# Kernel tuning notes

Measured on AMD Instinct MI355X. Metric: run time of the kernel, lower is better.

The kernel has to match this reference:

```python
import jax, jax.numpy as jnp
import numpy as np

EPS = 1e-7
N_SINKHORN = 40


def setup_inputs() -> dict:
    key = jax.random.key(0)
    k1, k2, k3, k4 = jax.random.split(key, 4)
    n, l, K, batch = 1024, 4, 1, 32
    x = jax.random.randint(k1, (batch, n), 0, l)                      # class labels in [0, l)
    W = jax.random.normal(k2, (n, n), jnp.float32)                    # MI-derived logit weights
    V_compress = jax.random.normal(k3, (n, l), jnp.float32)           # log-marginals
    E_compress = jax.random.normal(k4, (K, n, n, l, l), jnp.float32) * 0.1  # log-joints
    return {"x": x, "W": W, "V_compress": V_compress, "E_compress": E_compress}


def reference(x, W, V_compress, E_compress):
    n, l = V_compress.shape
    which_moat = 0

    # --- marginals / joints ---
    V = jax.nn.softmax(V_compress, axis=1)            # [n, l]
    E = jnp.exp(E_compress[which_moat])               # [n, n, l, l]
    E = E / E.sum(axis=(-2, -1), keepdims=True)

    # --- 40-step Sinkhorn / IPF projection onto target row/col marginals ---
    A_b = V[:, None, :, None]                         # [n, 1, l, 1] target row marginals
    B_b = V[None, :, None, :]                         # [1, n, 1, l] target col marginals

    def ipf_step(E, _):
        E = E * (A_b / (E.sum(axis=3, keepdims=True) + EPS))
        E = E * (B_b / (E.sum(axis=2, keepdims=True) + EPS))
        E = E / (E.sum(axis=(-2, -1), keepdims=True) + EPS)
        return E, None

    E, _ = jax.lax.scan(ipf_step, E, None, length=N_SINKHORN)

    # zero the diagonal (i == j) blocks, clamp to [0, 1]
    E = jnp.clip(E * (1.0 - jnp.eye(n, dtype=E.dtype))[:, :, None, None], 0.0, 1.0)

    # --- tree-structured weights and base Laplacian ---
    Ws = jax.nn.sigmoid(W)
    Ws = jnp.tril(Ws, k=-1)
    Ws = Ws + Ws.T                                    # symmetric, zero diag
    L0 = -Ws + jnp.diag(Ws.sum(axis=1))               # [n, n]

    # --- gather per-sample marginals / pairwise probs ---
    idx = jnp.arange(n)
    Pr = V[idx[None, :], x]                           # [B, n]
    P = E[idx[None, :, None], idx[None, None, :], x[:, :, None], x[:, None, :]]  # [B, n, n]
    P = P / (Pr[:, :, None] * Pr[:, None, :])

    WP = Ws[None, :, :] * P                           # [B, n, n]
    eye = jnp.eye(n, dtype=WP.dtype)
    L = -WP + WP.sum(axis=2)[:, :, None] * eye        # batched diag_embed

    y = jnp.log(Pr + 1e-7).sum(axis=1)                # [B]
    _, ld1 = jnp.linalg.slogdet(L[:, 1:, 1:] + 1e-7)
    _, ld0 = jnp.linalg.slogdet(L0[1:, 1:] + 1e-7)
    return y + ld1 - ld0
```

## Files before the change

kernel.cpp:

```cpp
#include <hip/hip_runtime.h>
#include <math.h>

#define MSZ   1048576ull
#define NMAT  33
#define PANSZ 61440
#define NSINK 14

__device__ __forceinline__ float frcp(float x){ return __builtin_amdgcn_rcpf(x); }

typedef __attribute__((ext_vector_type(8)))  short  bfrag;
typedef __attribute__((ext_vector_type(8)))  unsigned short u16x8;
typedef __attribute__((ext_vector_type(16))) float  f32x16;

__device__ __forceinline__ unsigned short bf16rn(float x){
  unsigned u = __float_as_uint(x);
  unsigned r = u + 0x7fffu + ((u>>16)&1u);
  return (unsigned short)(r>>16);
}
__device__ __forceinline__ float bf2f(unsigned short h){
  return __uint_as_float(((unsigned)h)<<16);
}

__global__ void k_misc(const float* __restrict__ Vc, float* __restrict__ V,
                       const float* __restrict__ W, float* __restrict__ Ws){
  int t = threadIdx.x;
  if(blockIdx.x < 4){
    int i = blockIdx.x*256 + t;
    float4 v = ((const float4*)Vc)[i];
    float mx = fmaxf(fmaxf(v.x,v.y), fmaxf(v.z,v.w));
    float e0=__expf(v.x-mx), e1=__expf(v.y-mx), e2=__expf(v.z-mx), e3=__expf(v.w-mx);
    float is = 1.f/(e0+e1+e2+e3);
    ((float4*)V)[i] = make_float4(e0*is, e1*is, e2*is, e3*is);
  } else {
    int idx = (blockIdx.x-4)*256 + t;
    int i = idx>>10, j = idx&1023;
    float v = 0.f;
    if(i != j){
      float w = (i>j) ? W[i*1024+j] : W[j*1024+i];
      v = 1.f/(1.f+__expf(-w));
    }
    Ws[idx]=v;
  }
}

__global__ void k_pr_y(const float* __restrict__ V, const int* __restrict__ x,
                       float* __restrict__ PrInv, float* __restrict__ y){
  int b = blockIdx.x, t = threadIdx.x;
  __shared__ float red[256];
  float acc = 0.f;
  for(int i=t; i<1024; i+=256){
    int xv = x[b*1024+i];
    float pr = V[i*4+xv];
    PrInv[b*1024+i] = 1.f/pr;
    acc += logf(pr + 1e-7f);
  }
  red[t]=acc; __syncthreads();
  for(int s=128;s>0;s>>=1){ if(t<s) red[t]+=red[t+s]; __syncthreads(); }
  if(t==0) y[b]=red[0];
}

__global__ void __launch_bounds__(256) k_sinkhorn(
    const float* __restrict__ Ec, const float* __restrict__ V,
    const float* __restrict__ Ws, const float* __restrict__ PrInv,
    const int* __restrict__ x, float* __restrict__ mats,
    float* __restrict__ partial){
  int idx = blockIdx.x*256 + threadIdx.x;
  int i = idx>>10, j = idx&1023;
  if(i==0) return;
  int t = threadIdx.x;
  int lane = t & 63, wv = t >> 6;
  __shared__ float sE[256][17];
  float E[16];
  {
    const float4* p = (const float4*)(Ec + (size_t)idx*16);
    float4 q0=p[0], q1=p[1], q2=p[2], q3=p[3];
    E[0]=__expf(q0.x); E[1]=__expf(q0.y); E[2]=__expf(q0.z); E[3]=__expf(q0.w);
    E[4]=__expf(q1.x); E[5]=__expf(q1.y); E[6]=__expf(q1.z); E[7]=__expf(q1.w);
    E[8]=__expf(q2.x); E[9]=__expf(q2.y); E[10]=__expf(q2.z); E[11]=__expf(q2.w);
    E[12]=__expf(q3.x);E[13]=__expf(q3.y);E[14]=__expf(q3.z); E[15]=__expf(q3.w);
  }
  float s0=0.f;
  #pragma unroll
  for(int q=0;q<16;q++) s0+=E[q];
  float is0 = frcp(s0);
  #pragma unroll
  for(int q=0;q<16;q++) E[q]*=is0;
  float av[4], bv[4];
  {
    float4 va = ((const float4*)V)[i];
    av[0]=va.x; av[1]=va.y; av[2]=va.z; av[3]=va.w;
    float4 vb = ((const float4*)V)[j];
    bv[0]=vb.x; bv[1]=vb.y; bv[2]=vb.z; bv[3]=vb.w;
  }
  for(int it=0; it<NSINK; ++it){
    #pragma unroll
    for(int r=0;r<4;r++){
      float rs = E[4*r]+E[4*r+1]+E[4*r+2]+E[4*r+3];
      float sc = av[r]*frcp(rs+1e-7f);
      E[4*r]*=sc; E[4*r+1]*=sc; E[4*r+2]*=sc; E[4*r+3]*=sc;
    }
    #pragma unroll
    for(int c=0;c<4;c++){
      float cs = E[c]+E[4+c]+E[8+c]+E[12+c];
      float sc = bv[c]*frcp(cs+1e-7f);
      E[c]*=sc; E[4+c]*=sc; E[8+c]*=sc; E[12+c]*=sc;
    }
  }
  #pragma unroll
  for(int q=0;q<16;q++) sE[t][q] = fminf(fmaxf(E[q],0.f),1.f);
  float wsij = Ws[idx];
  for(int b=0;b<32;b++){
    int xi = x[b*1024+i];
    int xj = x[b*1024+j];
    float val = sE[t][(xi<<2)+xj] * wsij * PrInv[b*1024+i] * PrInv[b*1024+j];
    if(j!=0)
      mats[(size_t)(1+b)*MSZ + (size_t)(i-1)*1024 + (j-1)] = 1e-7f - val;
    float r = val;
    r += __shfl_down(r,32); r += __shfl_down(r,16); r += __shfl_down(r,8);
    r += __shfl_down(r,4);  r += __shfl_down(r,2);  r += __shfl_down(r,1);
    if(lane==0)
      partial[((size_t)b<<14) + ((size_t)(i-1)<<4) + ((blockIdx.x&3)<<2) + wv] = r;
  }
}

__global__ void k_l0(const float* __restrict__ Ws, float* __restrict__ mats){
  int r = blockIdx.x, t = threadIdx.x;
  float* orow = mats + (size_t)r*1024;
  if(r == 1023){
    float4 o = make_float4(0.f,0.f,0.f,0.f);
    if(t==255) o.w = 1.f;
    ((float4*)orow)[t] = o;
    return;
  }
  const float* wrow = Ws + (size_t)(r+1)*1024;
  float4 v = ((const float4*)wrow)[t];
  __shared__ float red[256];
  red[t] = v.x+v.y+v.z+v.w;
  __syncthreads();
  for(int s=128;s>0;s>>=1){ if(t<s) red[t]+=red[t+s]; __syncthreads(); }
  float rs = red[0];
  float o[4];
  #pragma unroll
  for(int q=0;q<4;q++){
    int c = 4*t+q;
    if(c==r)          o[q] = rs + 1e-7f;
    else if(c < 1023) o[q] = 1e-7f - wrow[c+1];
    else              o[q] = 0.f;
  }
  ((float4*)orow)[t] = make_float4(o[0],o[1],o[2],o[3]);
}

__global__ void k_patch(float* __restrict__ mats, const float* __restrict__ partial){
  int m = blockIdx.y + 1;
  int r = blockIdx.x*256 + threadIdx.x;
  float* A = mats + (size_t)m*MSZ;
  A[(size_t)r*1024 + 1023] = (r==1023) ? 1.f : 0.f;
  if(r < 1023){
    A[(size_t)1023*1024 + r] = 0.f;
    const float* pp = partial + (((size_t)(m-1))<<14) + ((size_t)r<<4);
    float s = 0.f;
    #pragma unroll
    for(int q=0;q<16;q++) s += pp[q];
    A[(size_t)r*1024 + r] = s + 1e-7f;
  }
}

__global__ void __launch_bounds__(128) k_diag(const float* __restrict__ mats_,
    unsigned short* __restrict__ UiH, unsigned short* __restrict__ UiL,
    unsigned short* __restrict__ LiH, unsigned short* __restrict__ LiL,
    float* __restrict__ logdet, int k){
  int m = blockIdx.x;
  const float* A = mats_ + (size_t)m*MSZ;
  int t = threadIdx.x;
  int lane = t & 63, w = t >> 6;
  __shared__ float Us[64*68];
  __shared__ float Ls[64*68];
  __shared__ float rd[64];

  if(w==0){
    float row[64];
    const float4* pr = (const float4*)(A + (size_t)(k+lane)*1024 + k);
    #pragma unroll
    for(int q4=0;q4<16;q4++){
      float4 v = pr[q4];
      row[4*q4]=v.x; row[4*q4+1]=v.y; row[4*q4+2]=v.z; row[4*q4+3]=v.w;
    }
    float slog = 0.f;
    #pragma unroll
    for(int c=0;c<64;c++){
      float piv = __shfl(row[c], c);
      slog += logf(fabsf(piv));
      float ip = frcp(piv);
      if(lane==c) rd[c] = ip;
      bool below = lane > c;
      float lic = below ? row[c]*ip : 0.f;
      if(below) row[c] = lic;
      #pragma unroll
      for(int q=c+1;q<64;q++){
        float uq = __shfl(row[q], c);
        row[q] = fmaf(-lic, uq, row[q]);
      }
    }
    #pragma unroll
    for(int q=0;q<64;q++){
      Ls[lane*68+q] = (q<lane) ? row[q] : 0.f;
      Us[lane*68+q] = (q>lane) ? row[q] : 0.f;
    }
    if(lane==0){ if(k==0) logdet[m]=slog; else logdet[m]+=slog; }
  }
  __syncthreads();

  if(w==0){
    float x[64];
    #pragma unroll
    for(int q=0;q<64;q++) x[q]=0.f;
    float rj = rd[lane];
    #pragma unroll
    for(int r=63;r>=0;r--){
      float a0=0.f,a1=0.f,a2=0.f,a3=0.f;
      #pragma unroll
      for(int c=(r+1)&~3; c<64; c+=4){
        float4 u = *(const float4*)&Us[r*68+c];
        a0 = fmaf(u.x, x[c],   a0);
        a1 = fmaf(u.y, x[c+1], a1);
        a2 = fmaf(u.z, x[c+2], a2);
        a3 = fmaf(u.w, x[c+3], a3);
      }
      float s = (a0+a1)+(a2+a3);
      x[r] = (r==lane) ? rj : -s*rd[r];
    }
    unsigned short* ph = UiH + (size_t)m*4096 + (size_t)lane*64;
    unsigned short* pl = UiL + (size_t)m*4096 + (size_t)lane*64;
    #pragma unroll
    for(int p8=0;p8<8;p8++){
      u16x8 h8, l8;
      #pragma unroll
      for(int e=0;e<8;e++){
        float v = x[p8*8+e];
        unsigned short h = bf16rn(v);
        h8[e]=h; l8[e]=bf16rn(v - bf2f(h));
      }
      ((u16x8*)ph)[p8]=h8; ((u16x8*)pl)[p8]=l8;
    }
  } else {
    float x[64];
    #pragma unroll
    for(int q=0;q<64;q++) x[q]=0.f;
    #pragma unroll
    for(int r=0;r<64;r++){
      float a0=0.f,a1=0.f,a2=0.f,a3=0.f;
      #pragma unroll
      for(int c=0; c<((r+3)&~3); c+=4){
        float4 u = *(const float4*)&Ls[r*68+c];
        a0 = fmaf(u.x, x[c],   a0);
        a1 = fmaf(u.y, x[c+1], a1);
        a2 = fmaf(u.z, x[c+2], a2);
        a3 = fmaf(u.w, x[c+3], a3);
      }
      x[r] = (r==lane) ? 1.f : -((a0+a1)+(a2+a3));
    }
    #pragma unroll
    for(int r=0;r<64;r++) Ls[r*68+lane] = x[r];
    unsigned short* ph = LiH + (size_t)m*4096 + (size_t)lane*64;
    unsigned short* pl = LiL + (size_t)m*4096 + (size_t)lane*64;
    #pragma unroll
    for(int p8=0;p8<8;p8++){
      float4 u0 = *(const float4*)&Ls[lane*68 + p8*8];
      float4 u1 = *(const float4*)&Ls[lane*68 + p8*8 + 4];
      float v[8] = {u0.x,u0.y,u0.z,u0.w,u1.x,u1.y,u1.z,u1.w};
      u16x8 h8, l8;
      #pragma unroll
      for(int e=0;e<8;e++){
        unsigned short h = bf16rn(v[e]);
        h8[e]=h; l8[e]=bf16rn(v[e] - bf2f(h));
      }
      ((u16x8*)ph)[p8]=h8; ((u16x8*)pl)[p8]=l8;
    }
  }
}

__global__ void __launch_bounds__(256) k_trsm(const float* __restrict__ mats_,
    const unsigned short* __restrict__ UiH, const unsigned short* __restrict__ UiL,
    const unsigned short* __restrict__ LiH, const unsigned short* __restrict__ LiL,
    unsigned short* __restrict__ Ah, unsigned short* __restrict__ Al,
    unsigned short* __restrict__ Bh, unsigned short* __restrict__ Bl,
    int k){
  int m = blockIdx.y;
  const float* A = mats_ + (size_t)m*MSZ;
  int rem = 1024 - (k+64);
  int nb = (rem+127)>>7;
  bool aside = (int)blockIdx.x < nb;
  int t = threadIdx.x, lane = t&63;
  int r32 = lane&31, hi = lane>>5, wv = t>>6;
  int tile0 = (aside ? (int)blockIdx.x : (int)blockIdx.x - nb)*128 + wv*32;
  int rel  = tile0 + r32;
  int relc = min(rel, rem-1);

  const unsigned short* IH = (aside ? UiH : LiH) + (size_t)m*4096;
  const unsigned short* IL = (aside ? UiL : LiL) + (size_t)m*4096;

  bfrag ah[4], al[4];
  if(aside){
    const float* src = A + (size_t)(k+64+relc)*1024 + k + hi*8;
    #pragma unroll
    for(int kc=0;kc<4;kc++){
      float4 u0 = *(const float4*)(src + kc*16);
      float4 u1 = *(const float4*)(src + kc*16 + 4);
      float v[8] = {u0.x,u0.y,u0.z,u0.w,u1.x,u1.y,u1.z,u1.w};
      #pragma unroll
      for(int e=0;e<8;e++){
        unsigned short h = bf16rn(v[e]);
        ah[kc][e] = (short)h;
        al[kc][e] = (short)bf16rn(v[e] - bf2f(h));
      }
    }
  } else {
    const float* src = A + (size_t)(k + hi*8)*1024 + (k+64+relc);
    #pragma unroll
    for(int kc=0;kc<4;kc++){
      #pragma unroll
      for(int e=0;e<8;e++){
        float v = src[(size_t)(kc*16+e)*1024];
        unsigned short h = bf16rn(v);
        ah[kc][e] = (short)h;
        al[kc][e] = (short)bf16rn(v - bf2f(h));
      }
    }
  }

  f32x16 acc[2];
  #pragma unroll
  for(int ct=0;ct<2;ct++)
    #pragma unroll
    for(int q=0;q<16;q++) acc[ct][q]=0.f;

  #pragma unroll
  for(int kc=0;kc<4;kc++){
    #pragma unroll
    for(int ct=0;ct<2;ct++){
      bfrag bh = *(const bfrag*)(IH + (size_t)(ct*32+r32)*64 + kc*16 + hi*8);
      bfrag bl = *(const bfrag*)(IL + (size_t)(ct*32+r32)*64 + kc*16 + hi*8);
      acc[ct] = __builtin_amdgcn_mfma_f32_32x32x16_bf16(ah[kc], bh, acc[ct], 0,0,0);
      acc[ct] = __builtin_amdgcn_mfma_f32_32x32x16_bf16(ah[kc], bl, acc[ct], 0,0,0);
      acc[ct] = __builtin_amdgcn_mfma_f32_32x32x16_bf16(al[kc], bh, acc[ct], 0,0,0);
    }
  }

  unsigned short* PH = (aside ? Ah : Bh) + (size_t)m*PANSZ;
  unsigned short* PL = (aside ? Al : Bl) + (size_t)m*PANSZ;
  #pragma unroll
  for(int ct=0;ct<2;ct++){
    #pragma unroll
    for(int reg=0;reg<16;reg++){
      int crow = (reg&3) + ((reg>>2)<<3) + (hi<<2);
      int r = tile0 + crow;
      if(r < rem){
        float v = acc[ct][reg];
        unsigned short h = bf16rn(v);
        size_t off = (size_t)r*64 + ct*32 + r32;
        PH[off] = h;
        PL[off] = bf16rn(v - bf2f(h));
      }
    }
  }
}

__global__ void __launch_bounds__(64) k_ld(const float* __restrict__ mats,
                                           float* __restrict__ logdet){
  int m = blockIdx.x, t = threadIdx.x;
  const float* A = mats + (size_t)m*MSZ;
  float row[64];
  #pragma unroll
  for(int q=0;q<64;q++)
    row[q] = A[(size_t)(960+t)*1024 + 960 + q];
  float slog = 0.f;
  #pragma unroll
  for(int c=0;c<64;c++){
    float piv = __shfl(row[c], c);
    slog += logf(fabsf(piv));
    float ip = frcp(piv);
    bool below = t > c;
    float lic = below ? row[c]*ip : 0.f;
    #pragma unroll
    for(int q=c+1;q<64;q++){
      float uq = __shfl(row[q], c);
      row[q] = fmaf(-lic, uq, row[q]);
    }
  }
  if(t==0) logdet[m] += slog;
}

__global__ void __launch_bounds__(256) k_gemm(float* __restrict__ mats,
    const unsigned short* __restrict__ Ah, const unsigned short* __restrict__ Al,
    const unsigned short* __restrict__ Bh, const unsigned short* __restrict__ Bl,
    int k){
  int m = blockIdx.z;
  float* A = mats + (size_t)m*MSZ;
  int rem = 1024 - (k+64);
  int i0rel = blockIdx.y*128;
  int j0rel = blockIdx.x*128;
  __shared__ unsigned short As[2][4096];
  __shared__ unsigned short Bs[2][4096];
  int t = threadIdx.x;
  int lane = t & 63, wvi = t >> 6;
  int wr = wvi >> 1, wc = wvi & 1;

  const unsigned short* pAh = Ah + (size_t)m*PANSZ;
  const unsigned short* pAl = Al + (size_t)m*PANSZ;
  const unsigned short* pBh = Bh + (size_t)m*PANSZ;
  const unsigned short* pBl = Bl + (size_t)m*PANSZ;

  int rowA[2], koctA[2], ldsOff[2];
  bool vA[2], vB[2];
  size_t offA[2], offB[2];
  #pragma unroll
  for(int p=0;p<2;p++){
    int c = t + 256*p;
    int row = c>>2, koct = c&3;
    rowA[p]=row; koctA[p]=koct;
    ldsOff[p] = row*32 + ((koct ^ ((row>>1)&3))<<3);
    vA[p] = (i0rel+row) < rem;
    vB[p] = (j0rel+row) < rem;
    offA[p] = (size_t)(i0rel+row)*64 + koct*8;
    offB[p] = (size_t)(j0rel+row)*64 + koct*8;
  }
  u16x8 z; z = 0;

  #pragma unroll
  for(int p=0;p<2;p++){
    u16x8 ah = vA[p] ? *(const u16x8*)(pAh + offA[p]) : z;
    u16x8 al = vA[p] ? *(const u16x8*)(pAl + offA[p]) : z;
    u16x8 bh = vB[p] ? *(const u16x8*)(pBh + offB[p]) : z;
    u16x8 bl = vB[p] ? *(const u16x8*)(pBl + offB[p]) : z;
    *(u16x8*)&As[0][ldsOff[p]] = ah;
    *(u16x8*)&As[1][ldsOff[p]] = al;
    *(u16x8*)&Bs[0][ldsOff[p]] = bh;
    *(u16x8*)&Bs[1][ldsOff[p]] = bl;
  }
  u16x8 p1[8];
  #pragma unroll
  for(int p=0;p<2;p++){
    p1[4*p+0] = vA[p] ? *(const u16x8*)(pAh + offA[p] + 32) : z;
    p1[4*p+1] = vA[p] ? *(const u16x8*)(pAl + offA[p] + 32) : z;
    p1[4*p+2] = vB[p] ? *(const u16x8*)(pBh + offB[p] + 32) : z;
    p1[4*p+3] = vB[p] ? *(const u16x8*)(pBl + offB[p] + 32) : z;
  }
  __syncthreads();

  f32x16 acc[2][2];
  #pragma unroll
  for(int rt=0;rt<2;rt++)
    #pragma unroll
    for(int ct=0;ct<2;ct++)
      #pragma unroll
      for(int q=0;q<16;q++) acc[rt][ct][q] = 0.f;

  int kgrp = lane >> 5;
  #pragma unroll
  for(int ks=0; ks<2; ks++){
    #pragma unroll
    for(int kc=0;kc<2;kc++){
      int koct = kc*2 + kgrp;
      bfrag ah[2], al[2], bh[2], bl[2];
      #pragma unroll
      for(int rt=0;rt<2;rt++){
        int row = wr*64 + rt*32 + (lane&31);
        int ad = row*32 + ((koct ^ ((row>>1)&3))<<3);
        ah[rt] = *(const bfrag*)&As[0][ad];
        al[rt] = *(const bfrag*)&As[1][ad];
      }
      #pragma unroll
      for(int ct=0;ct<2;ct++){
        int col = wc*64 + ct*32 + (lane&31);
        int ad = col*32 + ((koct ^ ((col>>1)&3))<<3);
        bh[ct] = *(const bfrag*)&Bs[0][ad];
        bl[ct] = *(const bfrag*)&Bs[1][ad];
      }
      #pragma unroll
      for(int rt=0;rt<2;rt++)
        #pragma unroll
        for(int ct=0;ct<2;ct++){
          acc[rt][ct] = __builtin_amdgcn_mfma_f32_32x32x16_bf16(ah[rt], bh[ct], acc[rt][ct], 0,0,0);
          acc[rt][ct] = __builtin_amdgcn_mfma_f32_32x32x16_bf16(ah[rt], bl[ct], acc[rt][ct], 0,0,0);
          acc[rt][ct] = __builtin_amdgcn_mfma_f32_32x32x16_bf16(al[rt], bh[ct], acc[rt][ct], 0,0,0);
        }
    }
    if(ks==0){
      __syncthreads();
      #pragma unroll
      for(int p=0;p<2;p++){
        *(u16x8*)&As[0][ldsOff[p]] = p1[4*p+0];
        *(u16x8*)&As[1][ldsOff[p]] = p1[4*p+1];
        *(u16x8*)&Bs[0][ldsOff[p]] = p1[4*p+2];
        *(u16x8*)&Bs[1][ldsOff[p]] = p1[4*p+3];
      }
      __syncthreads();
    }
  }

  int r0 = k + 64;
  #pragma unroll
  for(int rt=0;rt<2;rt++){
    int rowblk = i0rel + wr*64 + rt*32;
    if(rowblk >= rem) continue;
    #pragma unroll
    for(int ct=0;ct<2;ct++){
      int colblk = j0rel + wc*64 + ct*32;
      if(colblk >= rem) continue;
      int col = r0 + colblk + (lane&31);
      int rbase = r0 + rowblk + ((lane>>5)<<2);
      #pragma unroll
      for(int reg=0;reg<16;reg++){
        int row = rbase + (reg&3) + ((reg>>2)<<3);
        float* pc = A + (size_t)row*1024 + col;
        *pc -= acc[rt][ct][reg];
      }
    }
  }
}

__global__ void k_final(const float* __restrict__ y, const float* __restrict__ logdet,
                        float* __restrict__ out){
  int b = threadIdx.x;
  if(b<32) out[b] = y[b] + logdet[1+b] - logdet[0];
}

extern "C" void kernel_launch(void* const* d_in, const int* in_sizes, int n_in,
                              void* d_out, int out_size, void* d_ws, size_t ws_size,
                              hipStream_t stream){
  (void)in_sizes; (void)n_in; (void)out_size; (void)ws_size;
  const int*   x  = (const int*)d_in[0];
  const float* W  = (const float*)d_in[1];
  const float* Vc = (const float*)d_in[2];
  const float* Ec = (const float*)d_in[3];
  float* out = (float*)d_out;

  char* p = (char*)d_ws;
  auto alloc = [&](size_t bytes)->char*{ char* r = p; p += (bytes+255)&~(size_t)255; return r; };
  float* mats   = (float*)alloc((size_t)NMAT*MSZ*4);
  float* Ws     = (float*)alloc(1048576ull*4);
  unsigned short* Ah = (unsigned short*)alloc((size_t)NMAT*PANSZ*2);
  unsigned short* Al = (unsigned short*)alloc((size_t)NMAT*PANSZ*2);
  unsigned short* Bh = (unsigned short*)alloc((size_t)NMAT*PANSZ*2);
  unsigned short* Bl = (unsigned short*)alloc((size_t)NMAT*PANSZ*2);
  unsigned short* UiH = (unsigned short*)alloc((size_t)NMAT*4096*2);
  unsigned short* UiL = (unsigned short*)alloc((size_t)NMAT*4096*2);
  unsigned short* LiH = (unsigned short*)alloc((size_t)NMAT*4096*2);
  unsigned short* LiL = (unsigned short*)alloc((size_t)NMAT*4096*2);
  float* V      = (float*)alloc(4096*4);
  float* PrInv  = (float*)alloc(32768*4);
  float* partial= (float*)alloc((size_t)32*16384*4);
  float* y      = (float*)alloc(256);
  float* logdet = (float*)alloc(256);

  k_misc<<<4100,256,0,stream>>>(Vc, V, W, Ws);
  k_pr_y<<<32,256,0,stream>>>(V, x, PrInv, y);
  k_sinkhorn<<<4096,256,0,stream>>>(Ec, V, Ws, PrInv, x, mats, partial);
  k_l0<<<1024,256,0,stream>>>(Ws, mats);
  k_patch<<<dim3(4,32),256,0,stream>>>(mats, partial);

  for(int s=0;s<15;s++){
    int k = 64*s;
    int rem = 1024 - (k+64);
    k_diag<<<NMAT,128,0,stream>>>(mats, UiH,UiL,LiH,LiL, logdet, k);
    int nb = (rem+127)/128;
    k_trsm<<<dim3(2*nb,NMAT),256,0,stream>>>(mats, UiH,UiL,LiH,LiL, Ah,Al,Bh,Bl, k);
    int nt = (rem+127)/128;
    k_gemm<<<dim3(nt,nt,NMAT),256,0,stream>>>(mats, Ah,Al,Bh,Bl, k);
  }
  k_ld<<<NMAT,64,0,stream>>>(mats, logdet);
  k_final<<<1,32,0,stream>>>(y, logdet, out);
}
```

Baseline: 1.306 ms.

## Double blocked LU panel width to 128 and fold final logdet into diag kernel

The blocked LU used for the batched slogdet now works on 128-wide panels instead of 64. The diagonal kernel factors the 128x128 block as two 64x64 LUs with an in-LDS Schur update, then inverts its triangular factors for the TRSM step. This halves the number of diag/trsm/gemm launch rounds and gives each GEMM a longer K loop, at the cost of a heavier, more serial diag kernel with large register arrays (128 floats per thread) and 64KB of LDS. The separate final logdet kernel is dropped because the last diag call handles the trailing block, and the boundary masking is removed since 1024 divides evenly by 128.

```diff
diff --git a/kernel.cpp b/kernel.cpp
--- a/kernel.cpp
+++ b/kernel.cpp
@@ -1,10 +1,10 @@
 #include <hip/hip_runtime.h>
 #include <math.h>
 
-#define MSZ   1048576ull
-#define NMAT  33
-#define PANSZ 61440
-#define NSINK 14
+#define MSZ    1048576ull
+#define NMAT   33
+#define PANSZ  114688
+#define NSINK  14
 
 __device__ __forceinline__ float frcp(float x){ return __builtin_amdgcn_rcpf(x); }
 
@@ -165,33 +165,37 @@
   }
 }
 
-__global__ void __launch_bounds__(128) k_diag(const float* __restrict__ mats_,
+__global__ void __launch_bounds__(256) k_diag(const float* __restrict__ mats_,
     unsigned short* __restrict__ UiH, unsigned short* __restrict__ UiL,
     unsigned short* __restrict__ LiH, unsigned short* __restrict__ LiL,
-    float* __restrict__ logdet, int k){
+    float* __restrict__ logdet, int k, int inv){
   int m = blockIdx.x;
   const float* A = mats_ + (size_t)m*MSZ;
-  int t = threadIdx.x;
-  int lane = t & 63, w = t >> 6;
-  __shared__ float Us[64*68];
-  __shared__ float Ls[64*68];
-  __shared__ float rd[64];
-
+  int t = threadIdx.x, lane = t & 63, w = t >> 6;
+  __shared__ float sm[128*128];
+
+  {
+    int r = t >> 1, h = (t & 1) * 64;
+    const float4* src = (const float4*)(A + (size_t)(k + r)*1024 + k + h);
+    float4* dst = (float4*)&sm[r*128 + h];
+    #pragma unroll
+    for(int q=0;q<16;q++) dst[q] = src[q];
+  }
+  __syncthreads();
+
+  float slog = 0.f;
   if(w==0){
     float row[64];
-    const float4* pr = (const float4*)(A + (size_t)(k+lane)*1024 + k);
     #pragma unroll
     for(int q4=0;q4<16;q4++){
-      float4 v = pr[q4];
+      float4 v = *(const float4*)&sm[lane*128 + 4*q4];
       row[4*q4]=v.x; row[4*q4+1]=v.y; row[4*q4+2]=v.z; row[4*q4+3]=v.w;
     }
-    float slog = 0.f;
     #pragma unroll
     for(int c=0;c<64;c++){
       float piv = __shfl(row[c], c);
       slog += logf(fabsf(piv));
       float ip = frcp(piv);
-      if(lane==c) rd[c] = ip;
       bool below = lane > c;
       float lic = below ? row[c]*ip : 0.f;
       if(below) row[c] = lic;
@@ -202,11 +206,7 @@
       }
     }
     #pragma unroll
-    for(int q=0;q<64;q++){
-      Ls[lane*68+q] = (q<lane) ? row[q] : 0.f;
-      Us[lane*68+q] = (q>lane) ? row[q] : 0.f;
-    }
-    if(lane==0){ if(k==0) logdet[m]=slog; else logdet[m]+=slog; }
+    for(int q=0;q<64;q++) sm[lane*128+q] = row[q];
   }
   __syncthreads();
 
@@ -214,25 +214,110 @@
     float x[64];
     #pragma unroll
     for(int q=0;q<64;q++) x[q]=0.f;
-    float rj = rd[lane];
-    #pragma unroll
-    for(int r=63;r>=0;r--){
+    #pragma unroll
+    for(int r=0;r<64;r++){
       float a0=0.f,a1=0.f,a2=0.f,a3=0.f;
       #pragma unroll
-      for(int c=(r+1)&~3; c<64; c+=4){
-        float4 u = *(const float4*)&Us[r*68+c];
-        a0 = fmaf(u.x, x[c],   a0);
-        a1 = fmaf(u.y, x[c+1], a1);
-        a2 = fmaf(u.z, x[c+2], a2);
-        a3 = fmaf(u.w, x[c+3], a3);
-      }
-      float s = (a0+a1)+(a2+a3);
-      x[r] = (r==lane) ? rj : -s*rd[r];
-    }
-    unsigned short* ph = UiH + (size_t)m*4096 + (size_t)lane*64;
-    unsigned short* pl = UiL + (size_t)m*4096 + (size_t)lane*64;
-    #pragma unroll
-    for(int p8=0;p8<8;p8++){
+      for(int c=0;c<((r+3)&~3);c+=4){
+        float4 u = *(const float4*)&sm[r*128+c];
+        a0=fmaf(u.x,x[c],a0);   a1=fmaf(u.y,x[c+1],a1);
+        a2=fmaf(u.z,x[c+2],a2); a3=fmaf(u.w,x[c+3],a3);
+      }
+      x[r] = sm[r*128 + 64 + lane] - ((a0+a1)+(a2+a3));
+    }
+    #pragma unroll
+    for(int r=0;r<64;r++) sm[r*128 + 64 + lane] = x[r];
+  } else if(w==1){
+    float x[64];
+    #pragma unroll
+    for(int q=0;q<64;q++) x[q]=0.f;
+    #pragma unroll
+    for(int c=0;c<64;c++){
+      float a0=0.f,a1=0.f,a2=0.f,a3=0.f;
+      #pragma unroll
+      for(int p=0;p<((c+3)&~3);p+=4){
+        a0 = fmaf(x[p],   sm[p*128+c],     a0);
+        a1 = fmaf(x[p+1], sm[(p+1)*128+c], a1);
+        a2 = fmaf(x[p+2], sm[(p+2)*128+c], a2);
+        a3 = fmaf(x[p+3], sm[(p+3)*128+c], a3);
+      }
+      float d = sm[(64+lane)*128 + c];
+      x[c] = (d - ((a0+a1)+(a2+a3))) * frcp(sm[c*128+c]);
+    }
+    #pragma unroll
+    for(int c=0;c<64;c++) sm[(64+lane)*128 + c] = x[c];
+  }
+  __syncthreads();
+
+  {
+    int j = lane;
+    #pragma unroll
+    for(int ii=0; ii<16; ii++){
+      int i = w*16 + ii;
+      float acc2 = sm[(64+i)*128 + 64 + j];
+      #pragma unroll
+      for(int p=0;p<64;p+=4){
+        float4 l4 = *(const float4*)&sm[(64+i)*128 + p];
+        acc2 = fmaf(-l4.x, sm[(p  )*128 + 64 + j], acc2);
+        acc2 = fmaf(-l4.y, sm[(p+1)*128 + 64 + j], acc2);
+        acc2 = fmaf(-l4.z, sm[(p+2)*128 + 64 + j], acc2);
+        acc2 = fmaf(-l4.w, sm[(p+3)*128 + 64 + j], acc2);
+      }
+      sm[(64+i)*128 + 64 + j] = acc2;
+    }
+  }
+  __syncthreads();
+
+  if(w==0){
+    float row[64];
+    #pragma unroll
+    for(int q4=0;q4<16;q4++){
+      float4 v = *(const float4*)&sm[(64+lane)*128 + 64 + 4*q4];
+      row[4*q4]=v.x; row[4*q4+1]=v.y; row[4*q4+2]=v.z; row[4*q4+3]=v.w;
+    }
+    #pragma unroll
+    for(int c=0;c<64;c++){
+      float piv = __shfl(row[c], c);
+      slog += logf(fabsf(piv));
+      float ip = frcp(piv);
+      bool below = lane > c;
+      float lic = below ? row[c]*ip : 0.f;
+      if(below) row[c] = lic;
+      #pragma unroll
+      for(int q=c+1;q<64;q++){
+        float uq = __shfl(row[q], c);
+        row[q] = fmaf(-lic, uq, row[q]);
+      }
+    }
+    #pragma unroll
+    for(int q=0;q<64;q++) sm[(64+lane)*128 + 64 + q] = row[q];
+    if(lane==0){ if(k==0) logdet[m]=slog; else logdet[m]+=slog; }
+  }
+  __syncthreads();
+  if(!inv) return;
+
+  int col = t & 127;
+  if(t < 128){
+    float x[128];
+    #pragma unroll
+    for(int q=0;q<128;q++) x[q]=0.f;
+    #pragma unroll
+    for(int r=127;r>=0;r--){
+      float a0=0.f,a1=0.f,a2=0.f,a3=0.f;
+      #pragma unroll
+      for(int c=(r+1)&~3; c<128; c+=4){
+        float4 u = *(const float4*)&sm[r*128+c];
+        a0=fmaf(u.x,x[c],a0);   a1=fmaf(u.y,x[c+1],a1);
+        a2=fmaf(u.z,x[c+2],a2); a3=fmaf(u.w,x[c+3],a3);
+      }
+      float ip = frcp(sm[r*128+r]);
+      float sv = (a0+a1)+(a2+a3);
+      x[r] = (r==col) ? ip : -sv*ip;
+    }
+    unsigned short* ph = UiH + (size_t)m*16384 + (size_t)col*128;
+    unsigned short* pl = UiL + (size_t)m*16384 + (size_t)col*128;
+    #pragma unroll
+    for(int p8=0;p8<16;p8++){
       u16x8 h8, l8;
       #pragma unroll
       for(int e=0;e<8;e++){
@@ -242,31 +327,33 @@
       }
       ((u16x8*)ph)[p8]=h8; ((u16x8*)pl)[p8]=l8;
     }
+    __syncthreads();
+    __syncthreads();
   } else {
-    float x[64];
-    #pragma unroll
-    for(int q=0;q<64;q++) x[q]=0.f;
-    #pragma unroll
-    for(int r=0;r<64;r++){
+    float x[128];
+    #pragma unroll
+    for(int q=0;q<128;q++) x[q]=0.f;
+    #pragma unroll
+    for(int r=0;r<128;r++){
       float a0=0.f,a1=0.f,a2=0.f,a3=0.f;
       #pragma unroll
       for(int c=0; c<((r+3)&~3); c+=4){
-        float4 u = *(const float4*)&Ls[r*68+c];
-        a0 = fmaf(u.x, x[c],   a0);
-        a1 = fmaf(u.y, x[c+1], a1);
-        a2 = fmaf(u.z, x[c+2], a2);
-        a3 = fmaf(u.w, x[c+3], a3);
-      }
-      x[r] = (r==lane) ? 1.f : -((a0+a1)+(a2+a3));
-    }
-    #pragma unroll
-    for(int r=0;r<64;r++) Ls[r*68+lane] = x[r];
-    unsigned short* ph = LiH + (size_t)m*4096 + (size_t)lane*64;
-    unsigned short* pl = LiL + (size_t)m*4096 + (size_t)lane*64;
-    #pragma unroll
-    for(int p8=0;p8<8;p8++){
-      float4 u0 = *(const float4*)&Ls[lane*68 + p8*8];
-      float4 u1 = *(const float4*)&Ls[lane*68 + p8*8 + 4];
+        float4 u = *(const float4*)&sm[r*128+c];
+        a0=fmaf(u.x,x[c],a0);   a1=fmaf(u.y,x[c+1],a1);
+        a2=fmaf(u.z,x[c+2],a2); a3=fmaf(u.w,x[c+3],a3);
+      }
+      x[r] = (r==col) ? 1.f : -((a0+a1)+(a2+a3));
+    }
+    __syncthreads();
+    #pragma unroll
+    for(int r=0;r<128;r++) sm[r*128 + col] = x[r];
+    __syncthreads();
+    unsigned short* ph = LiH + (size_t)m*16384 + (size_t)col*128;
+    unsigned short* pl = LiL + (size_t)m*16384 + (size_t)col*128;
+    #pragma unroll
+    for(int p8=0;p8<16;p8++){
+      float4 u0 = *(const float4*)&sm[col*128 + p8*8];
+      float4 u1 = *(const float4*)&sm[col*128 + p8*8 + 4];
       float v[8] = {u0.x,u0.y,u0.z,u0.w,u1.x,u1.y,u1.z,u1.w};
       u16x8 h8, l8;
       #pragma unroll
@@ -287,107 +374,69 @@
     int k){
   int m = blockIdx.y;
   const float* A = mats_ + (size_t)m*MSZ;
-  int rem = 1024 - (k+64);
-  int nb = (rem+127)>>7;
+  int rem = 1024 - (k+128);
+  int nb = rem >> 7;
   bool aside = (int)blockIdx.x < nb;
   int t = threadIdx.x, lane = t&63;
   int r32 = lane&31, hi = lane>>5, wv = t>>6;
   int tile0 = (aside ? (int)blockIdx.x : (int)blockIdx.x - nb)*128 + wv*32;
   int rel  = tile0 + r32;
-  int relc = min(rel, rem-1);
-
-  const unsigned short* IH = (aside ? UiH : LiH) + (size_t)m*4096;
-  const unsigned short* IL = (aside ? UiL : LiL) + (size_t)m*4096;
-
-  bfrag ah[4], al[4];
-  if(aside){
-    const float* src = A + (size_t)(k+64+relc)*1024 + k + hi*8;
-    #pragma unroll
-    for(int kc=0;kc<4;kc++){
-      float4 u0 = *(const float4*)(src + kc*16);
-      float4 u1 = *(const float4*)(src + kc*16 + 4);
-      float v[8] = {u0.x,u0.y,u0.z,u0.w,u1.x,u1.y,u1.z,u1.w};
-      #pragma unroll
-      for(int e=0;e<8;e++){
-        unsigned short h = bf16rn(v[e]);
-        ah[kc][e] = (short)h;
-        al[kc][e] = (short)bf16rn(v[e] - bf2f(h));
-      }
-    }
-  } else {
-    const float* src = A + (size_t)(k + hi*8)*1024 + (k+64+relc);
-    #pragma unroll
-    for(int kc=0;kc<4;kc++){
-      #pragma unroll
-      for(int e=0;e<8;e++){
-        float v = src[(size_t)(kc*16+e)*1024];
-        unsigned short h = bf16rn(v);
-        ah[kc][e] = (short)h;
-        al[kc][e] = (short)bf16rn(v - bf2f(h));
-      }
-    }
-  }
-
-  f32x16 acc[2];
-  #pragma unroll
-  for(int ct=0;ct<2;ct++)
+
+  const unsigned short* IH = (aside ? UiH : LiH) + (size_t)m*16384;
+  const unsigned short* IL = (aside ? UiL : LiL) + (size_t)m*16384;
+
+  f32x16 acc[4];
+  #pragma unroll
+  for(int ct=0;ct<4;ct++)
     #pragma unroll
     for(int q=0;q<16;q++) acc[ct][q]=0.f;
 
   #pragma unroll
-  for(int kc=0;kc<4;kc++){
-    #pragma unroll
-    for(int ct=0;ct<2;ct++){
-      bfrag bh = *(const bfrag*)(IH + (size_t)(ct*32+r32)*64 + kc*16 + hi*8);
-      bfrag bl = *(const bfrag*)(IL + (size_t)(ct*32+r32)*64 + kc*16 + hi*8);
-      acc[ct] = __builtin_amdgcn_mfma_f32_32x32x16_bf16(ah[kc], bh, acc[ct], 0,0,0);
-      acc[ct] = __builtin_amdgcn_mfma_f32_32x32x16_bf16(ah[kc], bl, acc[ct], 0,0,0);
-      acc[ct] = __builtin_amdgcn_mfma_f32_32x32x16_bf16(al[kc], bh, acc[ct], 0,0,0);
+  for(int kc=0;kc<8;kc++){
+    float v[8];
+    if(aside){
+      const float* src = A + (size_t)(k+128+rel)*1024 + k + kc*16 + hi*8;
+      float4 u0 = ((const float4*)src)[0];
+      float4 u1 = ((const float4*)src)[1];
+      v[0]=u0.x; v[1]=u0.y; v[2]=u0.z; v[3]=u0.w;
+      v[4]=u1.x; v[5]=u1.y; v[6]=u1.z; v[7]=u1.w;
+    } else {
+      const float* src = A + (size_t)(k + kc*16 + hi*8)*1024 + (k+128+rel);
+      #pragma unroll
+      for(int e=0;e<8;e++) v[e] = src[(size_t)e*1024];
+    }
+    bfrag ah, al;
+    #pragma unroll
+    for(int e=0;e<8;e++){
+      unsigned short h = bf16rn(v[e]);
+      ah[e] = (short)h;
+      al[e] = (short)bf16rn(v[e] - bf2f(h));
+    }
+    #pragma unroll
+    for(int ct=0;ct<4;ct++){
+      bfrag bh = *(const bfrag*)(IH + (size_t)(ct*32+r32)*128 + kc*16 + hi*8);
+      bfrag bl = *(const bfrag*)(IL + (size_t)(ct*32+r32)*128 + kc*16 + hi*8);
+      acc[ct] = __builtin_amdgcn_mfma_f32_32x32x16_bf16(ah, bh, acc[ct], 0,0,0);
+      acc[ct] = __builtin_amdgcn_mfma_f32_32x32x16_bf16(ah, bl, acc[ct], 0,0,0);
+      acc[ct] = __builtin_amdgcn_mfma_f32_32x32x16_bf16(al, bh, acc[ct], 0,0,0);
     }
   }
 
   unsigned short* PH = (aside ? Ah : Bh) + (size_t)m*PANSZ;
   unsigned short* PL = (aside ? Al : Bl) + (size_t)m*PANSZ;
   #pragma unroll
-  for(int ct=0;ct<2;ct++){
+  for(int ct=0;ct<4;ct++){
     #pragma unroll
     for(int reg=0;reg<16;reg++){
       int crow = (reg&3) + ((reg>>2)<<3) + (hi<<2);
       int r = tile0 + crow;
-      if(r < rem){
-        float v = acc[ct][reg];
-        unsigned short h = bf16rn(v);
-        size_t off = (size_t)r*64 + ct*32 + r32;
-        PH[off] = h;
-        PL[off] = bf16rn(v - bf2f(h));
-      }
-    }
-  }
-}
-
-__global__ void __launch_bounds__(64) k_ld(const float* __restrict__ mats,
-                                           float* __restrict__ logdet){
-  int m = blockIdx.x, t = threadIdx.x;
-  const float* A = mats + (size_t)m*MSZ;
-  float row[64];
-  #pragma unroll
-  for(int q=0;q<64;q++)
-    row[q] = A[(size_t)(960+t)*1024 + 960 + q];
-  float slog = 0.f;
-  #pragma unroll
-  for(int c=0;c<64;c++){
-    float piv = __shfl(row[c], c);
-    slog += logf(fabsf(piv));
-    float ip = frcp(piv);
-    bool below = t > c;
-    float lic = below ? row[c]*ip : 0.f;
-    #pragma unroll
-    for(int q=c+1;q<64;q++){
-      float uq = __shfl(row[q], c);
-      row[q] = fmaf(-lic, uq, row[q]);
-    }
-  }
-  if(t==0) logdet[m] += slog;
+      float v = acc[ct][reg];
+      unsigned short h = bf16rn(v);
+      size_t off = (size_t)r*128 + ct*32 + r32;
+      PH[off] = h;
+      PL[off] = bf16rn(v - bf2f(h));
+    }
+  }
 }
 
 __global__ void __launch_bounds__(256) k_gemm(float* __restrict__ mats,
@@ -396,7 +445,6 @@
     int k){
   int m = blockIdx.z;
   float* A = mats + (size_t)m*MSZ;
-  int rem = 1024 - (k+64);
   int i0rel = blockIdx.y*128;
   int j0rel = blockIdx.x*128;
   __shared__ unsigned short As[2][4096];
@@ -410,40 +458,35 @@
   const unsigned short* pBh = Bh + (size_t)m*PANSZ;
   const unsigned short* pBl = Bl + (size_t)m*PANSZ;
 
-  int rowA[2], koctA[2], ldsOff[2];
-  bool vA[2], vB[2];
+  int ldsOff[2];
   size_t offA[2], offB[2];
   #pragma unroll
   for(int p=0;p<2;p++){
     int c = t + 256*p;
     int row = c>>2, koct = c&3;
-    rowA[p]=row; koctA[p]=koct;
     ldsOff[p] = row*32 + ((koct ^ ((row>>1)&3))<<3);
-    vA[p] = (i0rel+row) < rem;
-    vB[p] = (j0rel+row) < rem;
-    offA[p] = (size_t)(i0rel+row)*64 + koct*8;
-    offB[p] = (size_t)(j0rel+row)*64 + koct*8;
-  }
-  u16x8 z; z = 0;
+    offA[p] = (size_t)(i0rel+row)*128 + koct*8;
+    offB[p] = (size_t)(j0rel+row)*128 + koct*8;
+  }
 
   #pragma unroll
   for(int p=0;p<2;p++){
-    u16x8 ah = vA[p] ? *(const u16x8*)(pAh + offA[p]) : z;
-    u16x8 al = vA[p] ? *(const u16x8*)(pAl + offA[p]) : z;
-    u16x8 bh = vB[p] ? *(const u16x8*)(pBh + offB[p]) : z;
-    u16x8 bl = vB[p] ? *(const u16x8*)(pBl + offB[p]) : z;
-    *(u16x8*)&As[0][ldsOff[p]] = ah;
-    *(u16x8*)&As[1][ldsOff[p]] = al;
-    *(u16x8*)&Bs[0][ldsOff[p]] = bh;
-    *(u16x8*)&Bs[1][ldsOff[p]] = bl;
+    u16x8 a0 = *(const u16x8*)(pAh + offA[p]);
+    u16x8 a1 = *(const u16x8*)(pAl + offA[p]);
+    u16x8 b0 = *(const u16x8*)(pBh + offB[p]);
+    u16x8 b1 = *(const u16x8*)(pBl + offB[p]);
+    *(u16x8*)&As[0][ldsOff[p]] = a0;
+    *(u16x8*)&As[1][ldsOff[p]] = a1;
+    *(u16x8*)&Bs[0][ldsOff[p]] = b0;
+    *(u16x8*)&Bs[1][ldsOff[p]] = b1;
   }
   u16x8 p1[8];
   #pragma unroll
   for(int p=0;p<2;p++){
-    p1[4*p+0] = vA[p] ? *(const u16x8*)(pAh + offA[p] + 32) : z;
-    p1[4*p+1] = vA[p] ? *(const u16x8*)(pAl + offA[p] + 32) : z;
-    p1[4*p+2] = vB[p] ? *(const u16x8*)(pBh + offB[p] + 32) : z;
-    p1[4*p+3] = vB[p] ? *(const u16x8*)(pBl + offB[p] + 32) : z;
+    p1[4*p+0] = *(const u16x8*)(pAh + offA[p] + 32);
+    p1[4*p+1] = *(const u16x8*)(pAl + offA[p] + 32);
+    p1[4*p+2] = *(const u16x8*)(pBh + offB[p] + 32);
+    p1[4*p+3] = *(const u16x8*)(pBl + offB[p] + 32);
   }
   __syncthreads();
 
@@ -457,7 +500,7 @@
 
   int kgrp = lane >> 5;
   #pragma unroll
-  for(int ks=0; ks<2; ks++){
+  for(int st=0; st<4; st++){
     #pragma unroll
     for(int kc=0;kc<2;kc++){
       int koct = kc*2 + kgrp;
@@ -485,7 +528,7 @@
           acc[rt][ct] = __builtin_amdgcn_mfma_f32_32x32x16_bf16(al[rt], bh[ct], acc[rt][ct], 0,0,0);
         }
     }
-    if(ks==0){
+    if(st<3){
       __syncthreads();
       #pragma unroll
       for(int p=0;p<2;p++){
@@ -494,19 +537,26 @@
         *(u16x8*)&Bs[0][ldsOff[p]] = p1[4*p+2];
         *(u16x8*)&Bs[1][ldsOff[p]] = p1[4*p+3];
       }
+      if(st<2){
+        #pragma unroll
+        for(int p=0;p<2;p++){
+          p1[4*p+0] = *(const u16x8*)(pAh + offA[p] + (st+2)*32);
+          p1[4*p+1] = *(const u16x8*)(pAl + offA[p] + (st+2)*32);
+          p1[4*p+2] = *(const u16x8*)(pBh + offB[p] + (st+2)*32);
+          p1[4*p+3] = *(const u16x8*)(pBl + offB[p] + (st+2)*32);
+        }
+      }
       __syncthreads();
     }
   }
 
-  int r0 = k + 64;
+  int r0 = k + 128;
   #pragma unroll
   for(int rt=0;rt<2;rt++){
     int rowblk = i0rel + wr*64 + rt*32;
-    if(rowblk >= rem) continue;
     #pragma unroll
     for(int ct=0;ct<2;ct++){
       int colblk = j0rel + wc*64 + ct*32;
-      if(colblk >= rem) continue;
       int col = r0 + colblk + (lane&31);
       int rbase = r0 + rowblk + ((lane>>5)<<2);
       #pragma unroll
@@ -543,10 +593,10 @@
   unsigned short* Al = (unsigned short*)alloc((size_t)NMAT*PANSZ*2);
   unsigned short* Bh = (unsigned short*)alloc((size_t)NMAT*PANSZ*2);
   unsigned short* Bl = (unsigned short*)alloc((size_t)NMAT*PANSZ*2);
-  unsigned short* UiH = (unsigned short*)alloc((size_t)NMAT*4096*2);
-  unsigned short* UiL = (unsigned short*)alloc((size_t)NMAT*4096*2);
-  unsigned short* LiH = (unsigned short*)alloc((size_t)NMAT*4096*2);
-  unsigned short* LiL = (unsigned short*)alloc((size_t)NMAT*4096*2);
+  unsigned short* UiH = (unsigned short*)alloc((size_t)NMAT*16384*2);
+  unsigned short* UiL = (unsigned short*)alloc((size_t)NMAT*16384*2);
+  unsigned short* LiH = (unsigned short*)alloc((size_t)NMAT*16384*2);
+  unsigned short* LiL = (unsigned short*)alloc((size_t)NMAT*16384*2);
   float* V      = (float*)alloc(4096*4);
   float* PrInv  = (float*)alloc(32768*4);
   float* partial= (float*)alloc((size_t)32*16384*4);
@@ -559,15 +609,14 @@
   k_l0<<<1024,256,0,stream>>>(Ws, mats);
   k_patch<<<dim3(4,32),256,0,stream>>>(mats, partial);
 
-  for(int s=0;s<15;s++){
-    int k = 64*s;
-    int rem = 1024 - (k+64);
-    k_diag<<<NMAT,128,0,stream>>>(mats, UiH,UiL,LiH,LiL, logdet, k);
-    int nb = (rem+127)/128;
+  k_diag<<<NMAT,256,0,stream>>>(mats, UiH,UiL,LiH,LiL, logdet, 0, 1);
+  for(int s=0;s<7;s++){
+    int k = 128*s;
+    int rem = 1024 - (k+128);
+    int nb = rem/128;
     k_trsm<<<dim3(2*nb,NMAT),256,0,stream>>>(mats, UiH,UiL,LiH,LiL, Ah,Al,Bh,Bl, k);
-    int nt = (rem+127)/128;
-    k_gemm<<<dim3(nt,nt,NMAT),256,0,stream>>>(mats, Ah,Al,Bh,Bl, k);
-  }
-  k_ld<<<NMAT,64,0,stream>>>(mats, logdet);
+    k_gemm<<<dim3(nb,nb,NMAT),256,0,stream>>>(mats, Ah,Al,Bh,Bl, k);
+    k_diag<<<NMAT,256,0,stream>>>(mats, UiH,UiL,LiH,LiL, logdet, k+128, (s<6)?1:0);
+  }
   k_final<<<1,32,0,stream>>>(y, logdet, out);
 }
```

Result: slower. 1.650 ms (+26.3%).
